# Kernel tuning notes

Measured on AMD Instinct MI355X. Metric: run time of the kernel, lower is better.

The kernel has to match this reference:

```python
import jax, jax.numpy as jnp
import numpy as np

VOCAB = 5000
HID = 256
BATCH = 64
STEPS = 256


def setup_inputs() -> dict:
    key = jax.random.key(0)
    ks = jax.random.split(key, 7)
    scale_k = 1.0 / np.sqrt(VOCAB)
    scale_r = 1.0 / np.sqrt(HID)
    return {
        "tokens": jax.random.randint(ks[0], (BATCH, STEPS), 0, VOCAB, dtype=jnp.int32),
        "h0": jnp.zeros((BATCH, HID), dtype=jnp.float32),
        # GRUCell params (Keras reset_after=True layout): kernel [V,3H], recurrent [H,3H], bias [2,3H]
        "kernel": jax.random.normal(ks[1], (VOCAB, 3 * HID), dtype=jnp.float32) * scale_k,
        "rkernel": jax.random.normal(ks[2], (HID, 3 * HID), dtype=jnp.float32) * scale_r,
        "bias": jnp.zeros((2, 3 * HID), dtype=jnp.float32),
        # final Dense(vocab_size)
        "Wd": jax.random.normal(ks[3], (HID, VOCAB), dtype=jnp.float32) * scale_r,
        "bd": jnp.zeros((VOCAB,), dtype=jnp.float32),
    }


def reference(tokens, h0, kernel, rkernel, bias, Wd, bd):
    # X = one_hot(transpose(inputs), vocab)  -> time-major [T, B, V]
    X = jax.nn.one_hot(tokens.T, VOCAB, dtype=kernel.dtype)

    b_in, b_rec = bias[0], bias[1]

    def step(h, x):  # x: [B, V], h: [B, H]
        mx = x @ kernel + b_in            # [B, 3H]
        mh = h @ rkernel + b_rec          # [B, 3H]
        xz, xr, xh = jnp.split(mx, 3, axis=-1)
        hz, hr, hh = jnp.split(mh, 3, axis=-1)
        z = jax.nn.sigmoid(xz + hz)
        r = jax.nn.sigmoid(xr + hr)
        cand = jnp.tanh(xh + r * hh)      # reset_after=True candidate
        h_new = z * h + (1.0 - z) * cand
        return h_new, h_new

    h_last, Y = jax.lax.scan(step, h0, X)  # Y: [T, B, H]
    out = Y.reshape(-1, Y.shape[-1]) @ Wd + bd  # [T*B, V]
    return out, h_last
```

## Files before the change

kernel.cpp:

```cpp
#include <hip/hip_runtime.h>
#include <cstdint>

typedef __attribute__((ext_vector_type(8))) short bf16x8;
typedef __attribute__((ext_vector_type(4))) float f32x4;
typedef unsigned short u16;
typedef unsigned int u32;

#define T_STEPS 256
#define BATCH 64
#define HID 256
#define VOCAB 5000
#define KC 768
#define NWG 16
#define HB 16
#define NPAD 5120

__device__ __forceinline__ u16 f2bf(float x) {
  union { float f; u32 u; } v; v.f = x;
  u32 r = v.u + 0x7fffu + ((v.u >> 16) & 1u);
  return (u16)(r >> 16);
}
__device__ __forceinline__ float bf2f(u16 b) {
  union { float f; u32 u; } v; v.u = ((u32)b) << 16;
  return v.f;
}
__device__ __forceinline__ void load_lds16(const void* g, void* l) {
  __builtin_amdgcn_global_load_lds(
      (const __attribute__((address_space(1))) void*)g,
      (__attribute__((address_space(3))) void*)l, 16, 0, 0);
}

__global__ __launch_bounds__(256) void prep_b(const float* __restrict__ Wd,
                                              u16* __restrict__ BT) {
  int gid = blockIdx.x * 256 + threadIdx.x;
  int n = gid / 96;
  int k0 = (gid % 96) * 8;
  union { uint4 q; u16 s[8]; } o;
#pragma unroll
  for (int i = 0; i < 8; ++i) {
    int k = k0 + i;
    float x = 0.f;
    if (n < VOCAB) {
      int kk = (k < 512) ? (k & 255) : (k - 512);
      x = Wd[kk * VOCAB + n];
    }
    u16 hi = f2bf(x);
    o.s[i] = (k < 512) ? hi : f2bf(x - bf2f(hi));
  }
  *(uint4*)(BT + (size_t)n * KC + k0) = o.q;
}

__global__ __launch_bounds__(256) void prep_h0(const float* __restrict__ h0,
                                               u16* __restrict__ H0S) {
  int i = blockIdx.x * 256 + threadIdx.x;
  int b = i >> 8, j = i & 255;
  float x = h0[i];
  u16 hi = f2bf(x);
  u16 lo = f2bf(x - bf2f(hi));
  H0S[b * KC + j] = hi;
  H0S[b * KC + 256 + j] = lo;
}

__global__ __launch_bounds__(256, 1) void gru_rec(
    const int* __restrict__ tokens, const float* __restrict__ h0,
    const float* __restrict__ ker, const float* __restrict__ rker,
    const float* __restrict__ bias,
    u16* __restrict__ Abuf, const u16* __restrict__ H0S,
    float* __restrict__ hlast, u32* __restrict__ flags) {
  const int g = blockIdx.x;
  const int tid = threadIdx.x;
  const int w = tid >> 6;
  const int l = tid & 63;
  const int lm = l & 15;
  const int lq = l >> 4;

  int cmap[3]; float brec[3], bin[3];
#pragma unroll
  for (int nt = 0; nt < 3; ++nt) {
    cmap[nt] = nt * 256 + g * HB + lm;
    bin[nt]  = bias[cmap[nt]];
    brec[nt] = bias[KC + cmap[nt]];
  }

  bf16x8 Bhi[3][8], Blo[3][8];
#pragma unroll
  for (int nt = 0; nt < 3; ++nt)
#pragma unroll
    for (int kb = 0; kb < 8; ++kb) {
      union { bf16x8 v; u16 s[8]; } uh, ul;
#pragma unroll
      for (int jj = 0; jj < 8; ++jj) {
        int k = kb * 32 + lq * 8 + jj;
        float x = rker[k * KC + cmap[nt]];
        u16 hi = f2bf(x);
        uh.s[jj] = hi;
        ul.s[jj] = f2bf(x - bf2f(hi));
      }
      Bhi[nt][kb] = uh.v; Blo[nt][kb] = ul.v;
    }

  float hown[4];
#pragma unroll
  for (int r = 0; r < 4; ++r)
    hown[r] = h0[(16 * w + lq * 4 + r) * HID + g * HB + lm];

  const int rowloc = 16 * w + lm;

  for (int t = 0; t < T_STEPS; ++t) {
    float mx[3][4];
#pragma unroll
    for (int r = 0; r < 4; ++r) {
      int b = 16 * w + lq * 4 + r;
      int tok = tokens[b * T_STEPS + t];
#pragma unroll
      for (int nt = 0; nt < 3; ++nt)
        mx[nt][r] = ker[(size_t)tok * KC + cmap[nt]] + bin[nt];
    }

    if (t > 0) {
      const u32 tt = (u32)t;
      int guard = 0;
      for (;;) {
        u32 v = __hip_atomic_load(&flags[(l & 15) * 32], __ATOMIC_RELAXED,
                                  __HIP_MEMORY_SCOPE_AGENT);
        if (__all((int)(v >= tt))) break;
        if (++guard > (1 << 24)) break;
        __builtin_amdgcn_s_sleep(1);
      }
      __threadfence();
    }

    const u16* hsrc = (t == 0) ? H0S : (Abuf + (size_t)(t - 1) * BATCH * KC);
    const u16* hrow = hsrc + (size_t)rowloc * KC;
    bf16x8 Ahi[8], Alo[8];
#pragma unroll
    for (int kb = 0; kb < 8; ++kb) {
      union { uint4 q; bf16x8 v; } a0, a1;
      a0.q = *(const uint4*)(hrow + kb * 32 + lq * 8);
      a1.q = *(const uint4*)(hrow + 256 + kb * 32 + lq * 8);
      Ahi[kb] = a0.v; Alo[kb] = a1.v;
    }

    f32x4 acc[3];
#pragma unroll
    for (int nt = 0; nt < 3; ++nt)
      acc[nt] = (f32x4){brec[nt], brec[nt], brec[nt], brec[nt]};

#pragma unroll
    for (int kb = 0; kb < 8; ++kb) {
#pragma unroll
      for (int nt = 0; nt < 3; ++nt) {
        acc[nt] = __builtin_amdgcn_mfma_f32_16x16x32_bf16(Ahi[kb], Bhi[nt][kb], acc[nt], 0, 0, 0);
        acc[nt] = __builtin_amdgcn_mfma_f32_16x16x32_bf16(Alo[kb], Bhi[nt][kb], acc[nt], 0, 0, 0);
        acc[nt] = __builtin_amdgcn_mfma_f32_16x16x32_bf16(Ahi[kb], Blo[nt][kb], acc[nt], 0, 0, 0);
      }
    }

#pragma unroll
    for (int r = 0; r < 4; ++r) {
      float z  = 1.f / (1.f + expf(-(acc[0][r] + mx[0][r])));
      float rr = 1.f / (1.f + expf(-(acc[1][r] + mx[1][r])));
      float cd = tanhf(mx[2][r] + rr * acc[2][r]);
      float hn = z * hown[r] + (1.f - z) * cd;
      hown[r] = hn;
      u16 hi = f2bf(hn);
      u16 lo = f2bf(hn - bf2f(hi));
      int b = 16 * w + lq * 4 + r;
      u16* orow = Abuf + (size_t)(t * BATCH + b) * KC;
      orow[g * HB + lm]       = hi;
      orow[256 + g * HB + lm] = lo;
      orow[512 + g * HB + lm] = hi;
    }

    __threadfence();
    __syncthreads();
    if (tid == 0)
      __hip_atomic_store(&flags[g * 32], (u32)(t + 1), __ATOMIC_RELEASE,
                         __HIP_MEMORY_SCOPE_AGENT);
  }

#pragma unroll
  for (int r = 0; r < 4; ++r) {
    int b = 16 * w + lq * 4 + r;
    hlast[b * HID + g * HB + lm] = hown[r];
  }
}

__global__ __launch_bounds__(256, 2) void gemm_out(
    const u16* __restrict__ A, const u16* __restrict__ BT,
    const float* __restrict__ bd, float* __restrict__ out) {
  __shared__ u16 As[128 * 32];
  __shared__ u16 Bs[128 * 32];
  const int tid = threadIdx.x;
  const int w = tid >> 6, l = tid & 63;
  const int lm = l & 15, lq = l >> 4;
  const int wm = w & 1, wn = w >> 1;
  const int m0 = blockIdx.y * 128;
  const int n0 = blockIdx.x * 128;
  const int tr = tid >> 2;
  const int tc = (tid & 3) * 8;

  f32x4 acc[4][4] = {};

  for (int kb = 0; kb < 24; ++kb) {
    if (kb) __syncthreads();
#pragma unroll
    for (int j = 0; j < 2; ++j) {
      load_lds16(A  + (size_t)(m0 + j * 64 + tr) * KC + kb * 32 + tc,
                 As + j * 2048 + (tid >> 6) * 512);
      load_lds16(BT + (size_t)(n0 + j * 64 + tr) * KC + kb * 32 + tc,
                 Bs + j * 2048 + (tid >> 6) * 512);
    }
    __syncthreads();

    bf16x8 af[4], bfr[4];
#pragma unroll
    for (int mi = 0; mi < 4; ++mi)
      af[mi] = *(const bf16x8*)(As + (wm * 64 + mi * 16 + lm) * 32 + lq * 8);
#pragma unroll
    for (int ni = 0; ni < 4; ++ni)
      bfr[ni] = *(const bf16x8*)(Bs + (wn * 64 + ni * 16 + lm) * 32 + lq * 8);
#pragma unroll
    for (int mi = 0; mi < 4; ++mi)
#pragma unroll
      for (int ni = 0; ni < 4; ++ni)
        acc[mi][ni] = __builtin_amdgcn_mfma_f32_16x16x32_bf16(af[mi], bfr[ni], acc[mi][ni], 0, 0, 0);
  }

#pragma unroll
  for (int ni = 0; ni < 4; ++ni) {
    int n = n0 + wn * 64 + ni * 16 + lm;
    float bdv = (n < VOCAB) ? bd[n] : 0.f;
#pragma unroll
    for (int mi = 0; mi < 4; ++mi) {
#pragma unroll
      for (int r = 0; r < 4; ++r) {
        int m = m0 + wm * 64 + mi * 16 + lq * 4 + r;
        if (n < VOCAB) out[(size_t)m * VOCAB + n] = acc[mi][ni][r] + bdv;
      }
    }
  }
}

extern "C" void kernel_launch(void* const* d_in, const int* in_sizes, int n_in,
                              void* d_out, int out_size, void* d_ws, size_t ws_size,
                              hipStream_t stream) {
  const int*   tokens = (const int*)d_in[0];
  const float* h0     = (const float*)d_in[1];
  const float* ker    = (const float*)d_in[2];
  const float* rker   = (const float*)d_in[3];
  const float* bias   = (const float*)d_in[4];
  const float* Wd     = (const float*)d_in[5];
  const float* bd     = (const float*)d_in[6];
  float* out = (float*)d_out;
  char* ws = (char*)d_ws;

  u16* Abuf  = (u16*)(ws);
  u16* BT    = (u16*)(ws + 25165824);
  u16* H0S   = (u16*)(ws + 33030144);
  u32* flags = (u32*)(ws + 33128448);

  hipMemsetAsync(flags, 0, 2048, stream);
  prep_b<<<1920, 256, 0, stream>>>(Wd, BT);
  prep_h0<<<64, 256, 0, stream>>>(h0, H0S);
  gru_rec<<<NWG, 256, 0, stream>>>(tokens, h0, ker, rker, bias, Abuf, H0S,
                                   out + (size_t)16384 * VOCAB, flags);
  gemm_out<<<dim3(40, 128), 256, 0, stream>>>(Abuf, BT, bd, out);
}
```

Baseline: 2.299 ms.

## Use per-wave flags and coherent loads/stores to cut GRU step sync cost

Each wave now publishes its own progress flag (64 flags instead of 16), so the block-wide __syncthreads and the threadfences in the recurrent loop go away. h values are written with sc0 sc1 stores and read back with agent-scope atomic 64-bit loads, so other workgroups see them without full fences. Next-step tokens are prefetched, and sigmoid and tanh use fast exp and rcp intrinsics. The risks are weaker memory ordering (relaxed flag store after only an s_waitcnt), twice as many smaller loads, and slightly less accurate activations.

```diff
diff --git a/kernel.cpp b/kernel.cpp
--- a/kernel.cpp
+++ b/kernel.cpp
@@ -5,6 +5,7 @@
 typedef __attribute__((ext_vector_type(4))) float f32x4;
 typedef unsigned short u16;
 typedef unsigned int u32;
+typedef unsigned long long u64;
 
 #define T_STEPS 256
 #define BATCH 64
@@ -28,6 +29,18 @@
   __builtin_amdgcn_global_load_lds(
       (const __attribute__((address_space(1))) void*)g,
       (__attribute__((address_space(3))) void*)l, 16, 0, 0);
+}
+__device__ __forceinline__ void st_u16_coh(u16* p, u16 v) {
+  asm volatile("global_store_short %0, %1, off sc0 sc1" :: "v"(p), "v"((u32)v));
+}
+__device__ __forceinline__ u64 ld_u64_coh(const u16* p) {
+  return __hip_atomic_load((const u64*)p, __ATOMIC_RELAXED, __HIP_MEMORY_SCOPE_AGENT);
+}
+__device__ __forceinline__ float fsig(float x) {
+  return __builtin_amdgcn_rcpf(1.f + __expf(-x));
+}
+__device__ __forceinline__ float ftanh(float x) {
+  return 1.f - 2.f * __builtin_amdgcn_rcpf(1.f + __expf(2.f * x));
 }
 
 __global__ __launch_bounds__(256) void prep_b(const float* __restrict__ Wd,
@@ -106,28 +119,39 @@
 
   const int rowloc = 16 * w + lm;
 
+  int ntok[4];
+#pragma unroll
+  for (int r = 0; r < 4; ++r)
+    ntok[r] = tokens[(16 * w + lq * 4 + r) * T_STEPS];
+
   for (int t = 0; t < T_STEPS; ++t) {
+    int ctok[4];
+#pragma unroll
+    for (int r = 0; r < 4; ++r) ctok[r] = ntok[r];
+    if (t + 1 < T_STEPS) {
+#pragma unroll
+      for (int r = 0; r < 4; ++r)
+        ntok[r] = tokens[(16 * w + lq * 4 + r) * T_STEPS + t + 1];
+    }
+
     float mx[3][4];
 #pragma unroll
     for (int r = 0; r < 4; ++r) {
-      int b = 16 * w + lq * 4 + r;
-      int tok = tokens[b * T_STEPS + t];
 #pragma unroll
       for (int nt = 0; nt < 3; ++nt)
-        mx[nt][r] = ker[(size_t)tok * KC + cmap[nt]] + bin[nt];
+        mx[nt][r] = ker[(size_t)ctok[r] * KC + cmap[nt]] + bin[nt];
     }
 
     if (t > 0) {
       const u32 tt = (u32)t;
       int guard = 0;
       for (;;) {
-        u32 v = __hip_atomic_load(&flags[(l & 15) * 32], __ATOMIC_RELAXED,
+        u32 v = __hip_atomic_load(&flags[l * 32], __ATOMIC_RELAXED,
                                   __HIP_MEMORY_SCOPE_AGENT);
         if (__all((int)(v >= tt))) break;
         if (++guard > (1 << 24)) break;
         __builtin_amdgcn_s_sleep(1);
       }
-      __threadfence();
     }
 
     const u16* hsrc = (t == 0) ? H0S : (Abuf + (size_t)(t - 1) * BATCH * KC);
@@ -135,9 +159,13 @@
     bf16x8 Ahi[8], Alo[8];
 #pragma unroll
     for (int kb = 0; kb < 8; ++kb) {
-      union { uint4 q; bf16x8 v; } a0, a1;
-      a0.q = *(const uint4*)(hrow + kb * 32 + lq * 8);
-      a1.q = *(const uint4*)(hrow + 256 + kb * 32 + lq * 8);
+      union { u64 d[2]; bf16x8 v; } a0, a1;
+      const u16* p0 = hrow + kb * 32 + lq * 8;
+      const u16* p1 = hrow + 256 + kb * 32 + lq * 8;
+      a0.d[0] = ld_u64_coh(p0);
+      a0.d[1] = ld_u64_coh(p0 + 4);
+      a1.d[0] = ld_u64_coh(p1);
+      a1.d[1] = ld_u64_coh(p1 + 4);
       Ahi[kb] = a0.v; Alo[kb] = a1.v;
     }
 
@@ -158,25 +186,25 @@
 
 #pragma unroll
     for (int r = 0; r < 4; ++r) {
-      float z  = 1.f / (1.f + expf(-(acc[0][r] + mx[0][r])));
-      float rr = 1.f / (1.f + expf(-(acc[1][r] + mx[1][r])));
-      float cd = tanhf(mx[2][r] + rr * acc[2][r]);
+      float z  = fsig(acc[0][r] + mx[0][r]);
+      float rr = fsig(acc[1][r] + mx[1][r]);
+      float cd = ftanh(mx[2][r] + rr * acc[2][r]);
       float hn = z * hown[r] + (1.f - z) * cd;
       hown[r] = hn;
       u16 hi = f2bf(hn);
       u16 lo = f2bf(hn - bf2f(hi));
       int b = 16 * w + lq * 4 + r;
       u16* orow = Abuf + (size_t)(t * BATCH + b) * KC;
-      orow[g * HB + lm]       = hi;
-      orow[256 + g * HB + lm] = lo;
+      st_u16_coh(orow + g * HB + lm, hi);
+      st_u16_coh(orow + 256 + g * HB + lm, lo);
       orow[512 + g * HB + lm] = hi;
     }
 
-    __threadfence();
-    __syncthreads();
-    if (tid == 0)
-      __hip_atomic_store(&flags[g * 32], (u32)(t + 1), __ATOMIC_RELEASE,
+    asm volatile("s_waitcnt vmcnt(0)" ::: "memory");
+    if (l == 0)
+      __hip_atomic_store(&flags[(g * 4 + w) * 32], (u32)(t + 1), __ATOMIC_RELAXED,
                          __HIP_MEMORY_SCOPE_AGENT);
+    asm volatile("" ::: "memory");
   }
 
 #pragma unroll
@@ -260,7 +288,7 @@
   u16* H0S   = (u16*)(ws + 33030144);
   u32* flags = (u32*)(ws + 33128448);
 
-  hipMemsetAsync(flags, 0, 2048, stream);
+  hipMemsetAsync(flags, 0, 8192, stream);
   prep_b<<<1920, 256, 0, stream>>>(Wd, BT);
   prep_h0<<<64, 256, 0, stream>>>(h0, H0S);
   gru_rec<<<NWG, 256, 0, stream>>>(tokens, h0, ker, rker, bias, Abuf, H0S,
```

After: 2.254 ms. No clear change (-1.9%).
